# Kernel tuning notes

Measured on AMD Instinct MI355X. Metric: run time of the kernel, lower is better.

The kernel has to match this reference:

```python
import jax, jax.numpy as jnp
import numpy as np

B, H, L, D, S = 32, 1, 4096, 64, 512  # batch, heads(=1, codebook shared), seq, d_k, n_code
PE_LAM = 100000.0
EPS = 1e-6


def _sinusoid_embs(length, width, lam):
    # standard sinusoid table [length, width]: concat(sin, cos)
    pos = jnp.arange(length, dtype=jnp.float32)
    inv_lams = lam ** (-jnp.arange(0, width, 2, dtype=jnp.float32) / width)
    pre = pos[:, None] * inv_lams[None, :]
    return jnp.concatenate([jnp.sin(pre), jnp.cos(pre)], axis=-1)


def _codebook():
    # get_codebook: sinusoids -> rms-norm (center/gain/bias off) -> tau^{-1/2} scale -> stop-grad -> [1,S,D]
    c = _sinusoid_embs(S, D, PE_LAM)
    c = c * jax.lax.rsqrt(jnp.mean(jnp.square(c), axis=-1, keepdims=True) + EPS)
    tau = float(D) ** 0.5
    return jax.lax.stop_gradient((tau ** -0.5) * c)[None, ...]  # [H=1, S, D]


def setup_inputs() -> dict:
    key = jax.random.key(0)
    vecs = jax.random.normal(key, (B, H, L, D), dtype=jnp.float32)
    loss_mask = jnp.ones((B, L), dtype=jnp.float32)
    return {"vecs": vecs, "loss_mask": loss_mask}


def reference(vecs, loss_mask):
    c = _codebook()  # [1, S, D]
    # pairwise squared distances [B,H,L,S] via ||v||^2 - 2 v.c + ||c||^2
    diffs2 = (
        jnp.sum(jnp.square(vecs), axis=-1)[..., None]
        - 2.0 * jnp.einsum("bhlk,hsk->bhls", vecs, c)
        + jnp.sum(jnp.square(c), axis=-1)[None, :, None, :]
    )
    z = jnp.argmin(diffs2, axis=-1).astype(jnp.int32)       # [B,H,L]
    errs2 = jax.nn.relu(jnp.min(diffs2, axis=-1))           # [B,H,L]
    # gather codewords: codebook [1,1,S,D], indices [B,H,L,1]
    cz = jnp.take_along_axis(c[None, ...], z[..., None], axis=2)  # [B,H,L,D]
    # straight-through estimator
    quantized = jax.lax.stop_gradient(cz) + vecs - jax.lax.stop_gradient(vecs)
    # l_commit = mean over (B,L) of sum over heads of masked errs2
    l_commit = jnp.mean(jnp.sum(loss_mask[:, None, :] * errs2, axis=1))
    return quantized, z, l_commit, errs2
```

## Files before the change

kernel.cpp:

```cpp
#include <hip/hip_runtime.h>
#include <math.h>

#define NB 32
#define NL 4096
#define ND 64
#define NS 512
#define NTOK (NB*NL)

#define OFF_Q 0
#define OFF_Z (NTOK*ND)
#define OFF_LC (OFF_Z + NTOK)
#define OFF_E (OFF_LC + 1)

typedef __attribute__((ext_vector_type(8))) short short8;
typedef __attribute__((ext_vector_type(4))) float f32x4;
typedef unsigned int u32;
typedef unsigned short u16;
typedef unsigned long long u64;

#define QCODES 128
#define TOKS 256
#define TPB 256
#define SLOTS 16
#define SLOTP 17
#define EPS_H 1e-3f
#define NBLK (NTOK / TOKS)

__device__ __forceinline__ u32 f2bf_rne(float x) {
    u32 u = __float_as_uint(x);
    return (u + 0x7fffu + ((u >> 16) & 1u)) >> 16;
}

__device__ __forceinline__ void upd_key(u64& best, float dist, int code) {
    u32 u = __float_as_uint(dist);
    u ^= (u >> 31) ? 0xFFFFFFFFu : 0x80000000u;
    u64 k = ((u64)u << 32) | (u32)code;
    if (k < best) best = k;
}

__device__ __forceinline__ float dist_code(const float* __restrict__ cb,
                                           const float* __restrict__ ccs,
                                           const float4* vf, float vv, int code) {
    const float4* cs = (const float4*)(cb + (size_t)code * ND);
    float d0 = 0.f, d1 = 0.f, d2 = 0.f, d3 = 0.f;
    #pragma unroll
    for (int i = 0; i < 16; ++i) {
        float4 cv = cs[i];
        d0 = fmaf(cv.x, vf[i].x, d0);
        d1 = fmaf(cv.y, vf[i].y, d1);
        d2 = fmaf(cv.z, vf[i].z, d2);
        d3 = fmaf(cv.w, vf[i].w, d3);
    }
    float dot = (d0 + d1) + (d2 + d3);
    return (vv - 2.0f * dot) + ccs[code];
}

__global__ void cb_kernel(float* __restrict__ cb, float* __restrict__ cc,
                          u16* __restrict__ cbh, u16* __restrict__ cbl) {
    int s = blockIdx.x;
    int d = threadIdx.x;
    int j = (d < 32) ? d : (d - 32);
    double e = -(double)(2 * j) / 64.0;
    double invlam = pow(100000.0, e);
    double pre = (double)s * invlam;
    float val = (float)((d < 32) ? sin(pre) : cos(pre));

    float sq = val * val;
    #pragma unroll
    for (int off = 32; off > 0; off >>= 1) sq += __shfl_xor(sq, off);
    float mean = sq * (1.0f / 64.0f);
    float scale = (1.0f / sqrtf(mean + 1e-6f)) * 0.35355339059327379f;
    float c = val * scale;
    cb[s * ND + d] = c;

    float c2 = c * c;
    #pragma unroll
    for (int off = 32; off > 0; off >>= 1) c2 += __shfl_xor(c2, off);
    if (d == 0) cc[s] = c2;

    u32 hb = f2bf_rne(c);
    float hf = __uint_as_float(hb << 16);
    u32 lb = f2bf_rne(c - hf);
    int g = d >> 3, ee = d & 7;
    int pos = s * 64 + (((g ^ (s & 7)) << 3) | ee);
    cbh[pos] = (u16)hb;
    cbl[pos] = (u16)lb;
}

__launch_bounds__(TPB, 2)
__global__ void fused_kernel(const float* __restrict__ vecs,
                             const float* __restrict__ mask,
                             const float* __restrict__ cb,
                             const float* __restrict__ cc,
                             const u16* __restrict__ cbh,
                             const u16* __restrict__ cbl,
                             float* __restrict__ outq,
                             float* __restrict__ outz,
                             float* __restrict__ oute,
                             float* __restrict__ partial) {
    __shared__ u16 ldsH[QCODES * 64];
    __shared__ u16 ldsL[QCODES * 64];
    __shared__ u32 slots[TOKS * SLOTP];
    __shared__ float hval[TOKS * SLOTP];
    __shared__ float ccs[NS];
    __shared__ u32 cnt_l[TOKS];
    __shared__ int z_l[TOKS];
    __shared__ float wsum[TPB / 64];

    const int tid = threadIdx.x;
    const int grp = blockIdx.x;
    const int w = tid >> 6;
    const int lane = tid & 63;
    const int c16 = lane & 15;
    const int h = lane >> 4;

    #pragma unroll
    for (int i = 0; i < 4; ++i) {
        int k = i * TPB + tid;
        ((short8*)ldsH)[k] = ((const short8*)cbh)[k];
        ((short8*)ldsL)[k] = ((const short8*)cbl)[k];
    }
    ccs[tid] = cc[tid];
    ccs[tid + 256] = cc[tid + 256];
    cnt_l[tid] = 0;

    short8 bh[4][2], bl[4][2];
    const int tokbase = grp * TOKS + w * 64;
    #pragma unroll
    for (int nt = 0; nt < 4; ++nt) {
        const float* vp = vecs + (size_t)(tokbase + nt * 16 + c16) * ND;
        #pragma unroll
        for (int kk = 0; kk < 2; ++kk) {
            const float4* p = (const float4*)(vp + kk * 32 + h * 8);
            float4 t0 = p[0], t1 = p[1];
            float x[8] = {t0.x, t0.y, t0.z, t0.w, t1.x, t1.y, t1.z, t1.w};
            short8 H, L;
            #pragma unroll
            for (int e2 = 0; e2 < 8; ++e2) {
                u32 hb = f2bf_rne(x[e2]);
                float hf = __uint_as_float(hb << 16);
                u32 lb = f2bf_rne(x[e2] - hf);
                H[e2] = (short)hb; L[e2] = (short)lb;
            }
            bh[nt][kk] = H; bl[nt][kk] = L;
        }
    }
    __syncthreads();

    for (int q = 0; q < 4; ++q) {
        if (q) {
            __syncthreads();
            #pragma unroll
            for (int i = 0; i < 4; ++i) {
                int k = i * TPB + tid;
                ((short8*)ldsH)[k] = ((const short8*)(cbh + q * QCODES * 64))[k];
                ((short8*)ldsL)[k] = ((const short8*)(cbl + q * QCODES * 64))[k];
            }
            __syncthreads();
        }
        #pragma unroll
        for (int c = 0; c < 2; ++c) {
            f32x4 acc[4][4];
            #pragma unroll
            for (int mt = 0; mt < 4; ++mt) {
                int cr = q * QCODES + c * 64 + mt * 16 + h * 4;
                f32x4 ini;
                ini[0] = -0.5f * ccs[cr + 0];
                ini[1] = -0.5f * ccs[cr + 1];
                ini[2] = -0.5f * ccs[cr + 2];
                ini[3] = -0.5f * ccs[cr + 3];
                #pragma unroll
                for (int nt = 0; nt < 4; ++nt) acc[mt][nt] = ini;
            }
            #pragma unroll
            for (int mt = 0; mt < 4; ++mt) {
                int code_l = c * 64 + mt * 16 + c16;
                int sw = code_l & 7;
                short8 ah[2], al[2];
                #pragma unroll
                for (int kk = 0; kk < 2; ++kk) {
                    int off = code_l * 64 + (((kk * 4 + h) ^ sw) << 3);
                    ah[kk] = *(const short8*)(ldsH + off);
                    al[kk] = *(const short8*)(ldsL + off);
                }
                #pragma unroll
                for (int nt = 0; nt < 4; ++nt) {
                    #pragma unroll
                    for (int kk = 0; kk < 2; ++kk) {
                        acc[mt][nt] = __builtin_amdgcn_mfma_f32_16x16x32_bf16(ah[kk], bh[nt][kk], acc[mt][nt], 0, 0, 0);
                        acc[mt][nt] = __builtin_amdgcn_mfma_f32_16x16x32_bf16(ah[kk], bl[nt][kk], acc[mt][nt], 0, 0, 0);
                        acc[mt][nt] = __builtin_amdgcn_mfma_f32_16x16x32_bf16(al[kk], bh[nt][kk], acc[mt][nt], 0, 0, 0);
                    }
                }
            }
            #pragma unroll
            for (int nt = 0; nt < 4; ++nt) {
                float m = acc[0][nt][0];
                #pragma unroll
                for (int mt = 0; mt < 4; ++mt) {
                    m = fmaxf(m, fmaxf(fmaxf(acc[mt][nt][0], acc[mt][nt][1]),
                                       fmaxf(acc[mt][nt][2], acc[mt][nt][3])));
                }
                m = fmaxf(m, __shfl_xor(m, 16));
                m = fmaxf(m, __shfl_xor(m, 32));
                float thr = m - EPS_H;
                int tl = w * 64 + nt * 16 + c16;
                #pragma unroll
                for (int mt = 0; mt < 4; ++mt) {
                    #pragma unroll
                    for (int r = 0; r < 4; ++r) {
                        float v = acc[mt][nt][r];
                        if (v >= thr) {
                            u32 pos = atomicAdd(&cnt_l[tl], 1u);
                            if (pos < (u32)SLOTS) {
                                slots[tl * SLOTP + pos] = (u32)(q * QCODES + c * 64 + mt * 16 + h * 4 + r);
                                hval[tl * SLOTP + pos] = v;
                            }
                        }
                    }
                }
            }
        }
    }
    __syncthreads();

    const int p = tid;
    const int tok = grp * TOKS + p;

    float4 vf[16];
    {
        const float4* vr = (const float4*)(vecs + (size_t)tok * ND);
        #pragma unroll
        for (int g = 0; g < 16; ++g) vf[g] = vr[g];
    }
    float vv;
    {
        float a0 = 0.f, a1 = 0.f, a2 = 0.f, a3 = 0.f;
        #pragma unroll
        for (int i = 0; i < 16; ++i) {
            a0 = fmaf(vf[i].x, vf[i].x, a0);
            a1 = fmaf(vf[i].y, vf[i].y, a1);
            a2 = fmaf(vf[i].z, vf[i].z, a2);
            a3 = fmaf(vf[i].w, vf[i].w, a3);
        }
        vv = (a0 + a1) + (a2 + a3);
    }

    u64 best = 0xFFFFFFFFFFFFFFFFull;
    u32 cntraw = cnt_l[p];
    if (cntraw > (u32)SLOTS) {
        for (int code = 0; code < NS; ++code)
            upd_key(best, dist_code(cb, ccs, vf, vv, code), code);
    } else {
        float hm = -3.4e38f;
        for (u32 j2 = 0; j2 < cntraw; ++j2) hm = fmaxf(hm, hval[p * SLOTP + j2]);
        float thr2 = hm - EPS_H;
        for (u32 j2 = 0; j2 < cntraw; ++j2) {
            if (hval[p * SLOTP + j2] >= thr2) {
                int code = (int)slots[p * SLOTP + j2];
                upd_key(best, dist_code(cb, ccs, vf, vv, code), code);
            }
        }
    }

    int zi = (int)(best & 0xFFFFFFFFu);
    u32 du = (u32)(best >> 32);
    du ^= (du >> 31) ? 0x80000000u : 0xFFFFFFFFu;
    float dmin = __uint_as_float(du);
    float err = fmaxf(dmin, 0.0f);
    outz[tok] = (float)zi;
    oute[tok] = err;
    z_l[p] = zi;
    float contrib = mask[tok] * err;

    #pragma unroll
    for (int off = 32; off > 0; off >>= 1) contrib += __shfl_xor(contrib, off);
    if (lane == 0) wsum[w] = contrib;
    __syncthreads();
    if (tid == 0) {
        float t = 0.f;
        #pragma unroll
        for (int i = 0; i < TPB / 64; ++i) t += wsum[i];
        partial[grp] = t;
    }

    const float4* cb4 = (const float4*)cb;
    float4* qo = (float4*)(outq + (size_t)grp * TOKS * ND);
    #pragma unroll
    for (int i = 0; i < 16; ++i) {
        int gidx = i * TPB + tid;
        int t2 = gidx >> 4;
        int sub = gidx & 15;
        qo[gidx] = cb4[(size_t)z_l[t2] * 16 + sub];
    }
}

__global__ void fin_kernel(const float* __restrict__ partial, float* __restrict__ outl) {
    int t = threadIdx.x;
    float x = partial[t];
    #pragma unroll
    for (int off = 32; off > 0; off >>= 1) x += __shfl_xor(x, off);
    __shared__ float ws[8];
    if ((t & 63) == 0) ws[t >> 6] = x;
    __syncthreads();
    if (t == 0) {
        float s = 0.f;
        #pragma unroll
        for (int i = 0; i < 8; ++i) s += ws[i];
        outl[0] = s / (float)NTOK;
    }
}

extern "C" void kernel_launch(void* const* d_in, const int* in_sizes, int n_in,
                              void* d_out, int out_size, void* d_ws, size_t ws_size,
                              hipStream_t stream) {
    const float* vecs = (const float*)d_in[0];
    const float* mask = (const float*)d_in[1];

    float* out = (float*)d_out;
    float* outq = out + OFF_Q;
    float* outz = out + OFF_Z;
    float* outl = out + OFF_LC;
    float* oute = out + OFF_E;

    float* ws_f = (float*)d_ws;
    float* cb = ws_f;
    float* cc = ws_f + 32768;
    u16*  cbh = (u16*)(ws_f + 33280);
    u16*  cbl = (u16*)(ws_f + 49664);
    float* partial = ws_f + 66048;

    cb_kernel<<<NS, 64, 0, stream>>>(cb, cc, cbh, cbl);
    fused_kernel<<<NBLK, TPB, 0, stream>>>(vecs, mask, cb, cc, cbh, cbl,
                                           outq, outz, oute, partial);
    fin_kernel<<<1, 512, 0, stream>>>(partial, outl);
}
```

Before: 74.06 us.

## Stage full bf16 codebook in LDS and double tokens per block

Blocks now hold 512 tokens and 512 threads, and the whole split-bf16 codebook (hi and lo, 128 KB) is loaded into LDS once. This replaces the four quarter-codebook reloads and the barriers between them. The candidate slots shrink to u16 codes with no stored values, and the second-stage candidate filter is removed, so every candidate is rescored in fp32. Code norms are now read from global memory instead of LDS. The large LDS footprint limits occupancy to one block per CU and halves the grid to 256 blocks, and rescoring all candidates may add fp32 work.

```diff
diff --git a/kernel.cpp b/kernel.cpp
--- a/kernel.cpp
+++ b/kernel.cpp
@@ -18,13 +18,11 @@
 typedef unsigned short u16;
 typedef unsigned long long u64;
 
-#define QCODES 128
-#define TOKS 256
-#define TPB 256
+#define TOKS 512
+#define TPB 512
+#define NBLK (NTOK / TOKS)
 #define SLOTS 16
-#define SLOTP 17
 #define EPS_H 1e-3f
-#define NBLK (NTOK / TOKS)
 
 __device__ __forceinline__ u32 f2bf_rne(float x) {
     u32 u = __float_as_uint(x);
@@ -39,7 +37,7 @@
 }
 
 __device__ __forceinline__ float dist_code(const float* __restrict__ cb,
-                                           const float* __restrict__ ccs,
+                                           const float* __restrict__ cc,
                                            const float4* vf, float vv, int code) {
     const float4* cs = (const float4*)(cb + (size_t)code * ND);
     float d0 = 0.f, d1 = 0.f, d2 = 0.f, d3 = 0.f;
@@ -52,7 +50,7 @@
         d3 = fmaf(cv.w, vf[i].w, d3);
     }
     float dot = (d0 + d1) + (d2 + d3);
-    return (vv - 2.0f * dot) + ccs[code];
+    return (vv - 2.0f * dot) + cc[code];
 }
 
 __global__ void cb_kernel(float* __restrict__ cb, float* __restrict__ cc,
@@ -98,11 +96,9 @@
                              float* __restrict__ outz,
                              float* __restrict__ oute,
                              float* __restrict__ partial) {
-    __shared__ u16 ldsH[QCODES * 64];
-    __shared__ u16 ldsL[QCODES * 64];
-    __shared__ u32 slots[TOKS * SLOTP];
-    __shared__ float hval[TOKS * SLOTP];
-    __shared__ float ccs[NS];
+    __shared__ u16 ldsH[NS * 64];
+    __shared__ u16 ldsL[NS * 64];
+    __shared__ u16 slots[TOKS * SLOTS];
     __shared__ u32 cnt_l[TOKS];
     __shared__ int z_l[TOKS];
     __shared__ float wsum[TPB / 64];
@@ -115,13 +111,11 @@
     const int h = lane >> 4;
 
     #pragma unroll
-    for (int i = 0; i < 4; ++i) {
+    for (int i = 0; i < 8; ++i) {
         int k = i * TPB + tid;
         ((short8*)ldsH)[k] = ((const short8*)cbh)[k];
         ((short8*)ldsL)[k] = ((const short8*)cbl)[k];
     }
-    ccs[tid] = cc[tid];
-    ccs[tid + 256] = cc[tid + 256];
     cnt_l[tid] = 0;
 
     short8 bh[4][2], bl[4][2];
@@ -147,76 +141,62 @@
     }
     __syncthreads();
 
-    for (int q = 0; q < 4; ++q) {
-        if (q) {
-            __syncthreads();
-            #pragma unroll
-            for (int i = 0; i < 4; ++i) {
-                int k = i * TPB + tid;
-                ((short8*)ldsH)[k] = ((const short8*)(cbh + q * QCODES * 64))[k];
-                ((short8*)ldsL)[k] = ((const short8*)(cbl + q * QCODES * 64))[k];
-            }
-            __syncthreads();
-        }
-        #pragma unroll
-        for (int c = 0; c < 2; ++c) {
-            f32x4 acc[4][4];
-            #pragma unroll
-            for (int mt = 0; mt < 4; ++mt) {
-                int cr = q * QCODES + c * 64 + mt * 16 + h * 4;
-                f32x4 ini;
-                ini[0] = -0.5f * ccs[cr + 0];
-                ini[1] = -0.5f * ccs[cr + 1];
-                ini[2] = -0.5f * ccs[cr + 2];
-                ini[3] = -0.5f * ccs[cr + 3];
-                #pragma unroll
-                for (int nt = 0; nt < 4; ++nt) acc[mt][nt] = ini;
-            }
-            #pragma unroll
-            for (int mt = 0; mt < 4; ++mt) {
-                int code_l = c * 64 + mt * 16 + c16;
-                int sw = code_l & 7;
-                short8 ah[2], al[2];
+    for (int c = 0; c < 8; ++c) {
+        f32x4 acc[4][4];
+        #pragma unroll
+        for (int mt = 0; mt < 4; ++mt) {
+            int cr = c * 64 + mt * 16 + h * 4;
+            const float4 cv = *(const float4*)(cc + cr);
+            f32x4 ini;
+            ini[0] = -0.5f * cv.x;
+            ini[1] = -0.5f * cv.y;
+            ini[2] = -0.5f * cv.z;
+            ini[3] = -0.5f * cv.w;
+            #pragma unroll
+            for (int nt = 0; nt < 4; ++nt) acc[mt][nt] = ini;
+        }
+        #pragma unroll
+        for (int mt = 0; mt < 4; ++mt) {
+            int code_l = c * 64 + mt * 16 + c16;
+            int sw = code_l & 7;
+            short8 ah[2], al[2];
+            #pragma unroll
+            for (int kk = 0; kk < 2; ++kk) {
+                int off = code_l * 64 + (((kk * 4 + h) ^ sw) << 3);
+                ah[kk] = *(const short8*)(ldsH + off);
+                al[kk] = *(const short8*)(ldsL + off);
+            }
+            #pragma unroll
+            for (int nt = 0; nt < 4; ++nt) {
                 #pragma unroll
                 for (int kk = 0; kk < 2; ++kk) {
-                    int off = code_l * 64 + (((kk * 4 + h) ^ sw) << 3);
-                    ah[kk] = *(const short8*)(ldsH + off);
-                    al[kk] = *(const short8*)(ldsL + off);
+                    acc[mt][nt] = __builtin_amdgcn_mfma_f32_16x16x32_bf16(ah[kk], bh[nt][kk], acc[mt][nt], 0, 0, 0);
+                    acc[mt][nt] = __builtin_amdgcn_mfma_f32_16x16x32_bf16(ah[kk], bl[nt][kk], acc[mt][nt], 0, 0, 0);
+                    acc[mt][nt] = __builtin_amdgcn_mfma_f32_16x16x32_bf16(al[kk], bh[nt][kk], acc[mt][nt], 0, 0, 0);
                 }
+            }
+        }
+        #pragma unroll
+        for (int nt = 0; nt < 4; ++nt) {
+            float m = acc[0][nt][0];
+            #pragma unroll
+            for (int mt = 0; mt < 4; ++mt) {
+                m = fmaxf(m, fmaxf(fmaxf(acc[mt][nt][0], acc[mt][nt][1]),
+                                   fmaxf(acc[mt][nt][2], acc[mt][nt][3])));
+            }
+            m = fmaxf(m, __shfl_xor(m, 16));
+            m = fmaxf(m, __shfl_xor(m, 32));
+            float thr = m - EPS_H;
+            int tl = w * 64 + nt * 16 + c16;
+            #pragma unroll
+            for (int mt = 0; mt < 4; ++mt) {
                 #pragma unroll
-                for (int nt = 0; nt < 4; ++nt) {
-                    #pragma unroll
-                    for (int kk = 0; kk < 2; ++kk) {
-                        acc[mt][nt] = __builtin_amdgcn_mfma_f32_16x16x32_bf16(ah[kk], bh[nt][kk], acc[mt][nt], 0, 0, 0);
-                        acc[mt][nt] = __builtin_amdgcn_mfma_f32_16x16x32_bf16(ah[kk], bl[nt][kk], acc[mt][nt], 0, 0, 0);
-                        acc[mt][nt] = __builtin_amdgcn_mfma_f32_16x16x32_bf16(al[kk], bh[nt][kk], acc[mt][nt], 0, 0, 0);
-                    }
-                }
-            }
-            #pragma unroll
-            for (int nt = 0; nt < 4; ++nt) {
-                float m = acc[0][nt][0];
-                #pragma unroll
-                for (int mt = 0; mt < 4; ++mt) {
-                    m = fmaxf(m, fmaxf(fmaxf(acc[mt][nt][0], acc[mt][nt][1]),
-                                       fmaxf(acc[mt][nt][2], acc[mt][nt][3])));
-                }
-                m = fmaxf(m, __shfl_xor(m, 16));
-                m = fmaxf(m, __shfl_xor(m, 32));
-                float thr = m - EPS_H;
-                int tl = w * 64 + nt * 16 + c16;
-                #pragma unroll
-                for (int mt = 0; mt < 4; ++mt) {
-                    #pragma unroll
-                    for (int r = 0; r < 4; ++r) {
-                        float v = acc[mt][nt][r];
-                        if (v >= thr) {
-                            u32 pos = atomicAdd(&cnt_l[tl], 1u);
-                            if (pos < (u32)SLOTS) {
-                                slots[tl * SLOTP + pos] = (u32)(q * QCODES + c * 64 + mt * 16 + h * 4 + r);
-                                hval[tl * SLOTP + pos] = v;
-                            }
-                        }
+                for (int r = 0; r < 4; ++r) {
+                    float v = acc[mt][nt][r];
+                    if (v >= thr) {
+                        u32 pos = atomicAdd(&cnt_l[tl], 1u);
+                        if (pos < (u32)SLOTS)
+                            slots[tl * SLOTS + pos] = (u16)(c * 64 + mt * 16 + h * 4 + r);
                     }
                 }
             }
@@ -250,16 +230,11 @@
     u32 cntraw = cnt_l[p];
     if (cntraw > (u32)SLOTS) {
         for (int code = 0; code < NS; ++code)
-            upd_key(best, dist_code(cb, ccs, vf, vv, code), code);
+            upd_key(best, dist_code(cb, cc, vf, vv, code), code);
     } else {
-        float hm = -3.4e38f;
-        for (u32 j2 = 0; j2 < cntraw; ++j2) hm = fmaxf(hm, hval[p * SLOTP + j2]);
-        float thr2 = hm - EPS_H;
         for (u32 j2 = 0; j2 < cntraw; ++j2) {
-            if (hval[p * SLOTP + j2] >= thr2) {
-                int code = (int)slots[p * SLOTP + j2];
-                upd_key(best, dist_code(cb, ccs, vf, vv, code), code);
-            }
+            int code = (int)slots[p * SLOTS + j2];
+            upd_key(best, dist_code(cb, cc, vf, vv, code), code);
         }
     }
 
@@ -300,13 +275,13 @@
     float x = partial[t];
     #pragma unroll
     for (int off = 32; off > 0; off >>= 1) x += __shfl_xor(x, off);
-    __shared__ float ws[8];
+    __shared__ float ws[4];
     if ((t & 63) == 0) ws[t >> 6] = x;
     __syncthreads();
     if (t == 0) {
         float s = 0.f;
         #pragma unroll
-        for (int i = 0; i < 8; ++i) s += ws[i];
+        for (int i = 0; i < 4; ++i) s += ws[i];
         outl[0] = s / (float)NTOK;
     }
 }
@@ -333,5 +308,5 @@
     cb_kernel<<<NS, 64, 0, stream>>>(cb, cc, cbh, cbl);
     fused_kernel<<<NBLK, TPB, 0, stream>>>(vecs, mask, cb, cc, cbh, cbl,
                                            outq, outz, oute, partial);
-    fin_kernel<<<1, 512, 0, stream>>>(partial, outl);
-}
+    fin_kernel<<<1, 256, 0, stream>>>(partial, outl);
+}
```

After: 96.28 us. +30.0%, slower.
